# Performance work log

Hardware: AMD Instinct MI355X
Metric: run time of the kernel (lower is better)

The kernel has to match this reference:

```python
import jax, jax.numpy as jnp
import numpy as np
from jax import lax

B, T, A, L, H, FD = 32, 64, 6, 32, 128, 256


def setup_inputs() -> dict:
    key = jax.random.key(0)
    ks = jax.random.split(key, 24)
    rn = lambda k, s, sc: jax.random.normal(k, s, jnp.float32) * sc
    return {
        "states": rn(ks[0], (B, T, 3, 64, 64), 1.0),
        "actions": rn(ks[1], (B, T, A), 1.0),
        # CNN encoder params (scale ~ 1/sqrt(fan_in))
        "c1_w": rn(ks[2], (32, 3, 4, 4), 0.14), "c1_b": rn(ks[3], (32,), 0.01),
        "c2_w": rn(ks[4], (64, 32, 4, 4), 0.044), "c2_b": rn(ks[5], (64,), 0.01),
        "c3_w": rn(ks[6], (128, 64, 4, 4), 0.031), "c3_b": rn(ks[7], (128,), 0.01),
        "c4_w": rn(ks[8], (256, 128, 4, 4), 0.022), "c4_b": rn(ks[9], (256,), 0.01),
        "fc_w": rn(ks[10], (FD, 256 * 4 * 4), 0.0156), "fc_b": rn(ks[11], (FD,), 0.01),
        # GRUCell params (torch layout: W_ih (3H, in), W_hh (3H, H))
        "gru_wih": rn(ks[12], (3 * H, L + A), 0.16), "gru_whh": rn(ks[13], (3 * H, H), 0.088),
        "gru_bih": rn(ks[14], (3 * H,), 0.01), "gru_bhh": rn(ks[15], (3 * H,), 0.01),
        "prior_w": rn(ks[16], (2 * L, H), 0.088), "prior_b": rn(ks[17], (2 * L,), 0.01),
        "post_w": rn(ks[18], (2 * L, H + FD), 0.05), "post_b": rn(ks[19], (2 * L,), 0.01),
        # reparameterization noise (randn_like in torch), one per (b, t)
        "eps": rn(ks[20], (B, T, L), 1.0),
    }


def _conv(x, w, b):
    # Conv2d(k=4, stride=2, pad=1), NCHW/OIHW
    y = lax.conv_general_dilated(x, w, window_strides=(2, 2),
                                 padding=[(1, 1), (1, 1)],
                                 dimension_numbers=("NCHW", "OIHW", "NCHW"))
    return jax.nn.relu(y + b[None, :, None, None])


def _encode(x, c1_w, c1_b, c2_w, c2_b, c3_w, c3_b, c4_w, c4_b, fc_w, fc_b):
    # x: (N, 3, 64, 64) -> (N, FD)
    x = _conv(x, c1_w, c1_b)
    x = _conv(x, c2_w, c2_b)
    x = _conv(x, c3_w, c3_b)
    x = _conv(x, c4_w, c4_b)  # (N, 256, 4, 4)
    x = x.reshape(x.shape[0], -1)
    return x @ fc_w.T + fc_b


def _gru_cell(x, h, wih, whh, bih, bhh):
    gi = x @ wih.T + bih
    gh = h @ whh.T + bhh
    i_r, i_z, i_n = jnp.split(gi, 3, axis=-1)
    h_r, h_z, h_n = jnp.split(gh, 3, axis=-1)
    r = jax.nn.sigmoid(i_r + h_r)
    z = jax.nn.sigmoid(i_z + h_z)
    n = jnp.tanh(i_n + r * h_n)
    return (1.0 - z) * n + z * h


def reference(states, actions, c1_w, c1_b, c2_w, c2_b, c3_w, c3_b, c4_w, c4_b,
              fc_w, fc_b, gru_wih, gru_whh, gru_bih, gru_bhh,
              prior_w, prior_b, post_w, post_b, eps):
    b, t = states.shape[0], states.shape[1]
    # encoder has no recurrent dependency: encode all frames at once
    feats = _encode(states.reshape(b * t, *states.shape[2:]),
                    c1_w, c1_b, c2_w, c2_b, c3_w, c3_b, c4_w, c4_b,
                    fc_w, fc_b).reshape(b, t, -1)  # (B, T, FD)

    def step(carry, inp):
        h, z = carry
        a_t, f_t, e_t = inp
        h = _gru_cell(jnp.concatenate([z, a_t], -1), h,
                      gru_wih, gru_whh, gru_bih, gru_bhh)
        mu_p, lv_p = jnp.split(h @ prior_w.T + prior_b, 2, axis=-1)
        mu_q, lv_q = jnp.split(jnp.concatenate([h, f_t], -1) @ post_w.T + post_b, 2, axis=-1)
        z = mu_q + jnp.exp(0.5 * lv_q) * e_t
        return (h, z), (mu_p, lv_p, mu_q, lv_q, h, z)

    h0 = jnp.zeros((b, gru_whh.shape[1]), states.dtype)
    z0 = jnp.zeros((b, prior_w.shape[0] // 2), states.dtype)
    xs = (jnp.swapaxes(actions, 0, 1), jnp.swapaxes(feats, 0, 1),
          jnp.swapaxes(eps, 0, 1))
    _, ys = lax.scan(step, (h0, z0), xs)
    # (T, B, d) -> (B, T, d)
    return tuple(jnp.swapaxes(y, 0, 1) for y in ys)
```

## Files before the change

kernel.cpp:

```cpp
#include <hip/hip_runtime.h>
#include <math.h>

#define Bn 32
#define Tn 64
#define An 6
#define Ln 32
#define Hn 128
#define FDn 256
#define Nimg (Bn*Tn)

typedef __attribute__((ext_vector_type(8))) short frag_ab;
typedef __attribute__((ext_vector_type(4))) float frag_cd;
typedef _Float16 h2_t __attribute__((ext_vector_type(2)));

__device__ __forceinline__ float sigmoid_fast(float x){
  return __builtin_amdgcn_rcpf(1.f + __expf(-x));
}
__device__ __forceinline__ float tanh_fast(float x){
  float x2 = fminf(fmaxf(2.f*x, -30.f), 30.f);
  float e = __expf(x2);
  return (e - 1.f) * __builtin_amdgcn_rcpf(e + 1.f);
}

__device__ __forceinline__ unsigned short f2bf(float f){
  unsigned int u = __float_as_uint(f);
  unsigned int r = (u + 0x7fffu + ((u >> 16) & 1u)) >> 16;
  return (unsigned short)r;
}
__device__ __forceinline__ unsigned packh(float a, float b){
  union { h2_t h; unsigned u; } x;
  x.h = (h2_t){(_Float16)a, (_Float16)b};
  return x.u;
}
__device__ __forceinline__ float fdot2u(unsigned a, unsigned b, float c){
  union { unsigned u; h2_t h; } ua, ub;
  ua.u = a; ub.u = b;
#if __has_builtin(__builtin_amdgcn_fdot2)
  return __builtin_amdgcn_fdot2(ua.h, ub.h, c, false);
#else
  return c + (float)ua.h.x*(float)ub.h.x + (float)ua.h.y*(float)ub.h.y;
#endif
}
#define BAR_LDS() asm volatile("s_waitcnt lgkmcnt(0)\n\ts_barrier" ::: "memory")

__device__ __forceinline__ int swz_w(int r, int p){
  return ((r >> 4) << 9) + (p << 7) + ((((r & 15) ^ (p << 2))) << 3);
}
__device__ __forceinline__ int swz_r(int f, int l){
  return (f << 9) + ((l >> 4) << 7) + ((((l & 15) ^ ((l >> 4) << 2))) << 3);
}

__global__ void __launch_bounds__(256)
states_nhwc_kernel(const float* __restrict__ src, unsigned short* __restrict__ dst)
{
  int idx = blockIdx.x*256 + threadIdx.x;
  int n = idx >> 12, pix = idx & 4095;
  const float* s = src + (size_t)n*3*4096 + pix;
  union { unsigned short e[4]; uint2 v; } u;
  u.e[0] = f2bf(s[0]); u.e[1] = f2bf(s[4096]); u.e[2] = f2bf(s[8192]); u.e[3] = 0;
  *(uint2*)(dst + (size_t)idx*4) = u.v;
}

#define WHH4_U 24576
#define PO4_U  (64*53*4)
#define SCAN_U (WHH4_U + PO4_U)

__global__ void __launch_bounds__(256)
prep2_kernel(const float* __restrict__ c1w, const float* __restrict__ c2w,
             const float* __restrict__ c3w, const float* __restrict__ c4w,
             const float* __restrict__ fcw,
             const float* __restrict__ gwhh, const float* __restrict__ gwih,
             const float* __restrict__ prw,  const float* __restrict__ pow_,
             unsigned short* __restrict__ w1p, unsigned short* __restrict__ w2p,
             unsigned short* __restrict__ w3p, unsigned short* __restrict__ w4p,
             unsigned short* __restrict__ wfcp,
             unsigned* __restrict__ g_scan, unsigned* __restrict__ g_wih2,
             unsigned* __restrict__ g_pr2)
{
  const int bid = blockIdx.x, tid = threadIdx.x;
  if (bid < 128){
    int idx = bid*256+tid;
    int k = idx >> 9, r = idx & 511, tap = r >> 5, c = r & 31;
    w2p[idx] = f2bf(c2w[k*512 + c*16 + tap]);
  } else if (bid < 640){
    int idx = (bid-128)*256+tid;
    int k = idx >> 10, r = idx & 1023, tap = r >> 6, c = r & 63;
    w3p[idx] = f2bf(c3w[k*1024 + c*16 + tap]);
  } else if (bid < 2688){
    int idx = (bid-640)*256+tid;
    int k = idx >> 11, r = idx & 2047, tap = r >> 7, c = r & 127;
    w4p[idx] = f2bf(c4w[k*2048 + c*16 + tap]);
  } else if (bid < 6784){
    int idx = (bid-2688)*256+tid;
    int o = idx >> 12, r = idx & 4095, sp = r >> 8, c = r & 255;
    wfcp[idx] = f2bf(fcw[o*4096 + c*16 + sp]);
  } else if (bid < 6792){
    int idx = (bid-6784)*256+tid;
    int k = idx >> 6, r = idx & 63, tap = r >> 2, c = r & 3;
    w1p[idx] = (c < 3) ? f2bf(c1w[k*48 + c*16 + tap]) : (unsigned short)0;
  } else if (bid < 6888){
    int idx = (bid-6792)*256+tid;
    int q = idx & 3, r2 = idx >> 2;
    int k8 = r2 / 384, i = r2 - k8*384;
    int k = 8*k8 + 2*q;
    g_scan[idx] = packh(gwhh[i*128 + k], gwhh[i*128 + k + 1]);
  } else if (bid < 6917){
    int idx = (bid-6888)*256+tid;
    if (idx < 19*384){
      int c = idx / 384, i = idx - c*384;
      g_wih2[idx] = packh(gwih[i*38 + 2*c], gwih[i*38 + 2*c + 1]);
    }
  } else if (bid < 6933){
    int idx = (bid-6917)*256+tid;
    int o = idx >> 6, c = idx & 63;
    g_pr2[idx] = packh(prw[o*128 + 2*c], prw[o*128 + 2*c + 1]);
  } else {
    int idx = (bid-6933)*256+tid;
    if (idx < 64*192){
      int o = idx / 192, r2 = idx - o*192;
      int u = r2 >> 2, q = r2 & 3;
      int j = u / 12, kk = u - j*12;
      int k = 96*j + 8*kk + 2*q;
      g_scan[WHH4_U + (o*53 + j*13 + kk)*4 + q] =
        packh(pow_[o*384 + k], pow_[o*384 + k + 1]);
    }
  }
}

template<int Cin, int IN, int Kout, int OUT, int BN, int LOG_SPB>
__global__ void __launch_bounds__(256)
convN_mfma(const unsigned short* __restrict__ in,
           const unsigned short* __restrict__ wB,
           const float* __restrict__ bias,
           unsigned short* __restrict__ out)
{
  constexpr int SPB = OUT*OUT;
  constexpr int KD  = 16*Cin;
  constexpr int NCH = KD/32;
  constexpr int NFN = BN/32;
  constexpr int BFR = BN/16;
  constexpr int BSL = (BN*4 + 255)/256;
  __shared__ __align__(16) unsigned short Alds[2][8*512];
  __shared__ __align__(16) unsigned short Blds[2][BFR*512];

  const int tid = threadIdx.x;
  const int wave = tid >> 6, lane = tid & 63;
  const unsigned m0 = blockIdx.x * 128;
  const int n0 = blockIdx.y * BN;

  const int p = tid & 3;
  const unsigned short* baseA[2]; int oyA[2], oxA[2]; int AdstI[2];
#pragma unroll
  for (int h = 0; h < 2; h++){
    int r = (tid >> 2) + h*64;
    unsigned m = m0 + r;
    int nimg = m >> LOG_SPB;
    int sp = m & (SPB - 1);
    oyA[h] = sp / OUT; oxA[h] = sp & (OUT - 1);
    baseA[h] = in + (size_t)nimg * IN * IN * Cin;
    AdstI[h] = swz_w(r, p);
  }

  const unsigned short* BsrcH[BSL]; int BdstIH[BSL]; bool bActH[BSL];
#pragma unroll
  for (int h = 0; h < BSL; h++){
    int bn = (tid >> 2) + h*64, pb = tid & 3;
    bActH[h] = bn < BN;
    BsrcH[h] = wB + (size_t)(n0 + bn)*KD + pb*8;
    BdstIH[h] = swz_w(bn, pb);
  }

  const int mhalf = wave >> 1, nhalf = wave & 1;
  frag_cd acc[4][NFN];
#pragma unroll
  for (int i = 0; i < 4; i++)
#pragma unroll
    for (int j = 0; j < NFN; j++) acc[i][j] = (frag_cd){0.f,0.f,0.f,0.f};

  auto loadA = [&](int kt, int h) -> uint4 {
    if constexpr (Cin >= 32){
      constexpr int CPT = Cin/32;
      int tap = kt / CPT;
      int c0 = (kt - tap*CPT)*32;
      int kh = tap >> 2, kw = tap & 3;
      int iy = 2*oyA[h] - 1 + kh;
      int ix = 2*oxA[h] - 1 + kw;
      uint4 v = {0u,0u,0u,0u};
      if ((unsigned)iy < (unsigned)IN && (unsigned)ix < (unsigned)IN)
        v = *(const uint4*)(baseA[h] + ((iy*IN + ix)*Cin + c0 + p*8));
      return v;
    } else {
      int kh = kt*2 + (p >> 1);
      int kw0 = (p & 1)*2;
      int iy = 2*oyA[h] - 1 + kh;
      int ix0 = 2*oxA[h] - 1 + kw0;
      union { uint2 u2[2]; uint4 u4; } v; v.u4 = (uint4){0u,0u,0u,0u};
      bool iyok = (unsigned)iy < (unsigned)IN;
      const unsigned short* rowp = baseA[h] + iy*IN*4;
#pragma unroll
      for (int d = 0; d < 2; d++){
        int ix = ix0 + d;
        if (iyok && (unsigned)ix < (unsigned)IN) v.u2[d] = *(const uint2*)(rowp + ix*4);
      }
      return v.u4;
    }
  };

  const int rdoff = swz_r(0, lane);

  uint4 aR0 = loadA(0,0), aR1 = loadA(0,1);
  uint4 bR[BSL];
#pragma unroll
  for (int h = 0; h < BSL; h++)
    bR[h] = bActH[h] ? *(const uint4*)BsrcH[h] : (uint4){0u,0u,0u,0u};
  *(uint4*)&Alds[0][AdstI[0]] = aR0;
  *(uint4*)&Alds[0][AdstI[1]] = aR1;
#pragma unroll
  for (int h = 0; h < BSL; h++)
    if (bActH[h]) *(uint4*)&Blds[0][BdstIH[h]] = bR[h];
  if (NCH > 1){
    aR0 = loadA(1,0); aR1 = loadA(1,1);
#pragma unroll
    for (int h = 0; h < BSL; h++)
      if (bActH[h]) bR[h] = *(const uint4*)(BsrcH[h] + 32);
  }
  BAR_LDS();

#pragma unroll 2
  for (int kt = 0; kt < NCH; kt++){
    const int cur = kt & 1, nxt = cur ^ 1;
    if (kt + 1 < NCH){
      *(uint4*)&Alds[nxt][AdstI[0]] = aR0;
      *(uint4*)&Alds[nxt][AdstI[1]] = aR1;
#pragma unroll
      for (int h = 0; h < BSL; h++)
        if (bActH[h]) *(uint4*)&Blds[nxt][BdstIH[h]] = bR[h];
      if (kt + 2 < NCH){
        aR0 = loadA(kt+2, 0);
        aR1 = loadA(kt+2, 1);
#pragma unroll
        for (int h = 0; h < BSL; h++)
          if (bActH[h]) bR[h] = *(const uint4*)(BsrcH[h] + (kt+2)*32);
      }
    }
    frag_ab a[4], bf[NFN];
#pragma unroll
    for (int i = 0; i < 4; i++)
      a[i] = *(const frag_ab*)&Alds[cur][(((mhalf<<2) + i) << 9) + rdoff];
#pragma unroll
    for (int j = 0; j < NFN; j++)
      bf[j] = *(const frag_ab*)&Blds[cur][((nhalf*NFN + j) << 9) + rdoff];
#pragma unroll
    for (int i = 0; i < 4; i++)
#pragma unroll
      for (int j = 0; j < NFN; j++)
        acc[i][j] = __builtin_amdgcn_mfma_f32_16x16x32_bf16(a[i], bf[j], acc[i][j], 0, 0, 0);
    BAR_LDS();
  }

  const unsigned mb = m0 + mhalf*64 + ((lane >> 4) << 2);
#pragma unroll
  for (int j = 0; j < NFN; j++){
    const int kg = n0 + nhalf*(NFN*16) + j*16 + (lane & 15);
    const float bv = bias[kg];
#pragma unroll
    for (int i = 0; i < 4; i++){
#pragma unroll
      for (int r = 0; r < 4; r++){
        unsigned mg = mb + i*16 + r;
        out[(size_t)mg*Kout + kg] = f2bf(fmaxf(acc[i][j][r] + bv, 0.f));
      }
    }
  }
}

__global__ void __launch_bounds__(256)
fc_mfma2(const unsigned short* __restrict__ A, const unsigned short* __restrict__ wB,
         const float* __restrict__ bias, float* __restrict__ outF)
{
  constexpr int KD = 4096, NCH = KD/32;
  __shared__ __align__(16) unsigned short Alds[2][4*512];
  __shared__ __align__(16) unsigned short Blds[2][4*512];

  const int tid = threadIdx.x, wave = tid >> 6, lane = tid & 63;
  const int m0 = blockIdx.x * 64, n0 = blockIdx.y * 64;
  const int r = tid >> 2, pc = tid & 3;
  const unsigned short* Asrc = A + (size_t)(m0 + r)*KD + pc*8;
  const unsigned short* Bsrc = wB + (size_t)(n0 + r)*KD + pc*8;
  const int wI = swz_w(r, pc);
  const int mh = wave >> 1, nh = wave & 1;
  const int rdoff = swz_r(0, lane);

  frag_cd acc[2][2];
#pragma unroll
  for (int i = 0; i < 2; i++)
#pragma unroll
    for (int j = 0; j < 2; j++) acc[i][j] = (frag_cd){0.f,0.f,0.f,0.f};

  uint4 aP = *(const uint4*)Asrc, bP = *(const uint4*)Bsrc;
  *(uint4*)&Alds[0][wI] = aP;
  *(uint4*)&Blds[0][wI] = bP;
  aP = *(const uint4*)(Asrc + 32);
  bP = *(const uint4*)(Bsrc + 32);
  BAR_LDS();

#pragma unroll 2
  for (int kt = 0; kt < NCH; kt++){
    const int cur = kt & 1, nxt = cur ^ 1;
    if (kt + 1 < NCH){
      *(uint4*)&Alds[nxt][wI] = aP;
      *(uint4*)&Blds[nxt][wI] = bP;
      if (kt + 2 < NCH){
        aP = *(const uint4*)(Asrc + (kt+2)*32);
        bP = *(const uint4*)(Bsrc + (kt+2)*32);
      }
    }
    frag_ab a[2], b[2];
#pragma unroll
    for (int i = 0; i < 2; i++) a[i] = *(const frag_ab*)&Alds[cur][(((mh<<1)+i) << 9) + rdoff];
#pragma unroll
    for (int j = 0; j < 2; j++) b[j] = *(const frag_ab*)&Blds[cur][(((nh<<1)+j) << 9) + rdoff];
#pragma unroll
    for (int i = 0; i < 2; i++)
#pragma unroll
      for (int j = 0; j < 2; j++)
        acc[i][j] = __builtin_amdgcn_mfma_f32_16x16x32_bf16(a[i], b[j], acc[i][j], 0, 0, 0);
    BAR_LDS();
  }

  const int mb = m0 + mh*32 + ((lane >> 4) << 2);
#pragma unroll
  for (int j = 0; j < 2; j++){
    const int kg = n0 + nh*32 + j*16 + (lane & 15);
    const float bv = bias[kg];
#pragma unroll
    for (int i = 0; i < 2; i++)
#pragma unroll
      for (int rr = 0; rr < 4; rr++)
        outF[(size_t)(mb + i*16 + rr)*256 + kg] = acc[i][j][rr] + bv;
  }
}

__global__ void __launch_bounds__(384)
rssm_scan4(const float* __restrict__ actions, const float* __restrict__ feats,
           const float* __restrict__ eps,
           const unsigned* __restrict__ g_scan,
           const unsigned* __restrict__ g_wih2,
           const unsigned* __restrict__ g_pr2,
           const float* __restrict__ bih,  const float* __restrict__ bhh,
           const float* __restrict__ prior_b, const float* __restrict__ post_b,
           float* __restrict__ out)
{
  __shared__ __align__(16) _Float16 sh_hfh[384];
  __shared__ __align__(16) _Float16 sh_xh[40];
  __shared__ __align__(16) float sh_gi[384];
  __shared__ __align__(16) float sh_gh[384];

  const int b = blockIdx.x, tid = threadIdx.x;

  uint4 whhr[16];
  {
    const uint4* src = (const uint4*)g_scan;
#pragma unroll
    for (int k8 = 0; k8 < 16; k8++) whhr[k8] = src[k8*384 + tid];
  }
  unsigned wih[19];
#pragma unroll
  for (int c = 0; c < 19; c++) wih[c] = g_wih2[c*384 + tid];

  unsigned prw[32];
  float prb = 0.f;
  if (tid < 128){
    const unsigned* src = g_pr2 + (tid >> 1)*64 + (tid & 1)*32;
#pragma unroll
    for (int c = 0; c < 32; c++) prw[c] = src[c];
    prb = prior_b[tid >> 1];
  }

  int om = 0, pj = 0, o_p = 0; bool is_mu = false; float pob = 0.f;
  uint4 pww[12];
  if (tid >= 128){
    const int tt = tid - 128;
    om = tt >> 2; pj = tt & 3;
    o_p = (om >> 1) + (om & 1)*32;
    is_mu = !(om & 1);
    pob = post_b[o_p];
    const uint4* src = (const uint4*)(g_scan + WHH4_U) + o_p*53 + pj*13;
#pragma unroll
    for (int kk = 0; kk < 12; kk++) pww[kk] = src[kk];
  }

  const float bih_i = bih[tid], bhh_i = bhh[tid];
  float hreg = 0.f;

  {
    const int bt0 = b*Tn;
    if (tid < Hn) sh_hfh[tid] = (_Float16)0.f;
    if (tid < Ln) sh_xh[tid] = (_Float16)0.f;
    if (tid >= 32 && tid < 38) sh_xh[tid] = (_Float16)actions[(size_t)bt0*An + (tid-32)];
    if (tid >= 64 && tid < 320) sh_hfh[128 + tid - 64] = (_Float16)feats[(size_t)bt0*FDn + (tid-64)];
  }
  __syncthreads();

  const uint4* H4   = (const uint4*)sh_hfh;
  const unsigned* X2 = (const unsigned*)sh_xh;

  const int OFF_MUP = 0;
  const int OFF_LVP = Bn*Tn*Ln;
  const int OFF_MUQ = 2*Bn*Tn*Ln;
  const int OFF_LVQ = 3*Bn*Tn*Ln;
  const int OFF_H   = 4*Bn*Tn*Ln;
  const int OFF_Z   = 4*Bn*Tn*Ln + Bn*Tn*Hn;

  float freg = 0.f, areg = 0.f, epsr = 0.f;

  for (int t = 0; t < Tn; t++){
    const int bt = b*Tn + t;

    if (t > 0 && tid >= 64 && tid < 320) sh_hfh[128 + tid - 64] = (_Float16)freg;
    if (t < Tn-1){
      if (tid >= 64 && tid < 320) freg = feats[(size_t)(bt+1)*FDn + (tid-64)];
      if (tid >= 320 && tid < 326) areg = actions[(size_t)(bt+1)*An + (tid-320)];
    }
    if (tid >= 128 && ((tid-128)&7) == 0) epsr = eps[(size_t)bt*Ln + ((tid-128)>>3)];

    {
      float a0 = bih_i, a1 = 0.f;
#pragma unroll
      for (int c = 0; c < 19; c += 2) a0 = fdot2u(wih[c], X2[c], a0);
#pragma unroll
      for (int c = 1; c < 19; c += 2) a1 = fdot2u(wih[c], X2[c], a1);
      sh_gi[tid] = a0 + a1;

      float g0 = bhh_i, g1 = 0.f, g2 = 0.f, g3 = 0.f;
#pragma unroll
      for (int k8 = 0; k8 < 16; k8++){
        uint4 w = whhr[k8];
        uint4 h = H4[k8];
        g0 = fdot2u(w.x, h.x, g0);
        g1 = fdot2u(w.y, h.y, g1);
        g2 = fdot2u(w.z, h.z, g2);
        g3 = fdot2u(w.w, h.w, g3);
      }
      sh_gh[tid] = (g0 + g1) + (g2 + g3);
    }
    BAR_LDS();

    if (tid < Hn){
      const float r  = sigmoid_fast(sh_gi[tid]       + sh_gh[tid]);
      const float zg = sigmoid_fast(sh_gi[Hn  + tid] + sh_gh[Hn  + tid]);
      const float nn = tanh_fast(fmaf(r, sh_gh[2*Hn + tid], sh_gi[2*Hn + tid]));
      hreg = (1.f - zg)*nn + zg*hreg;
      sh_hfh[tid] = (_Float16)hreg;
      out[OFF_H + (size_t)bt*Hn + tid] = hreg;
    }
    if (t < Tn-1 && tid >= 320 && tid < 326) sh_xh[32 + tid - 320] = (_Float16)areg;
    BAR_LDS();

    if (tid < 128){
      const int j = tid & 1;
      float a0 = 0.f, a1 = 0.f, a2 = 0.f, a3 = 0.f;
#pragma unroll
      for (int c4 = 0; c4 < 8; c4++){
        uint4 h = H4[8*j + c4];
        a0 = fdot2u(prw[4*c4+0], h.x, a0);
        a1 = fdot2u(prw[4*c4+1], h.y, a1);
        a2 = fdot2u(prw[4*c4+2], h.z, a2);
        a3 = fdot2u(prw[4*c4+3], h.w, a3);
      }
      float p = (a0 + a1) + (a2 + a3);
      p += __shfl_xor(p, 1);
      if (j == 0){
        const int o = tid >> 1;
        p += prb;
        if (o < Ln) out[OFF_MUP + (size_t)bt*Ln + o] = p;
        else        out[OFF_LVP + (size_t)bt*Ln + (o - Ln)] = p;
      }
    } else {
      float a0 = 0.f, a1 = 0.f, a2 = 0.f, a3 = 0.f;
#pragma unroll
      for (int kk = 0; kk < 12; kk++){
        uint4 w = pww[kk];
        uint4 h = H4[pj*12 + kk];
        a0 = fdot2u(w.x, h.x, a0);
        a1 = fdot2u(w.y, h.y, a1);
        a2 = fdot2u(w.z, h.z, a2);
        a3 = fdot2u(w.w, h.w, a3);
      }
      float p = (a0 + a1) + (a2 + a3);
      p += __shfl_xor(p, 1);
      p += __shfl_xor(p, 2);
      p += pob;
      const float q_part = __shfl_xor(p, 4);
      if (pj == 0){
        if (is_mu){
          const int o = om >> 1;
          out[OFF_MUQ + (size_t)bt*Ln + o] = p;
          const float zz = fmaf(__expf(0.5f*q_part), epsr, p);
          sh_xh[o] = (_Float16)zz;
          out[OFF_Z + (size_t)bt*Ln + o] = zz;
        } else {
          out[OFF_LVQ + (size_t)bt*Ln + (o_p - Ln)] = p;
        }
      }
    }
    BAR_LDS();
  }
}

extern "C" void kernel_launch(void* const* d_in, const int* in_sizes, int n_in,
                              void* d_out, int out_size, void* d_ws, size_t ws_size,
                              hipStream_t stream)
{
  const float* states = (const float*)d_in[0];
  const float* actions= (const float*)d_in[1];
  const float* c1_w = (const float*)d_in[2];  const float* c1_b = (const float*)d_in[3];
  const float* c2_w = (const float*)d_in[4];  const float* c2_b = (const float*)d_in[5];
  const float* c3_w = (const float*)d_in[6];  const float* c3_b = (const float*)d_in[7];
  const float* c4_w = (const float*)d_in[8];  const float* c4_b = (const float*)d_in[9];
  const float* fc_w = (const float*)d_in[10]; const float* fc_b = (const float*)d_in[11];
  const float* gwih = (const float*)d_in[12]; const float* gwhh = (const float*)d_in[13];
  const float* gbih = (const float*)d_in[14]; const float* gbhh = (const float*)d_in[15];
  const float* pr_w = (const float*)d_in[16]; const float* pr_b = (const float*)d_in[17];
  const float* po_w = (const float*)d_in[18]; const float* po_b = (const float*)d_in[19];
  const float* eps  = (const float*)d_in[20];

  char* p = (char*)d_ws;
  auto alloc = [&](size_t bytes){ char* r = p; p += (bytes + 255) & ~255ULL; return r; };

  unsigned short* statesB = (unsigned short*)alloc((size_t)Nimg*4096*4*2);
  unsigned short* act1    = (unsigned short*)alloc((size_t)Nimg*1024*32*2);
  unsigned short* act2    = (unsigned short*)alloc((size_t)Nimg*256*64*2);
  unsigned short* act3    = (unsigned short*)alloc((size_t)Nimg*64*128*2);
  unsigned short* act4    = (unsigned short*)alloc((size_t)Nimg*16*256*2);
  float*          feats   = (float*)alloc((size_t)Nimg*FDn*4);
  unsigned short* w1p     = (unsigned short*)alloc(32*64*2);
  unsigned short* w2p     = (unsigned short*)alloc((size_t)64*512*2);
  unsigned short* w3p     = (unsigned short*)alloc((size_t)128*1024*2);
  unsigned short* w4p     = (unsigned short*)alloc((size_t)256*2048*2);
  unsigned short* wfcp    = (unsigned short*)alloc((size_t)256*4096*2);
  unsigned* g_scan = (unsigned*)alloc((size_t)SCAN_U*4);
  unsigned* g_wih2 = (unsigned*)alloc((size_t)19*384*4);
  unsigned* g_pr2  = (unsigned*)alloc((size_t)64*64*4);

  states_nhwc_kernel<<<Nimg*4096/256, 256, 0, stream>>>(states, statesB);
  prep2_kernel<<<6981, 256, 0, stream>>>(c1_w, c2_w, c3_w, c4_w, fc_w,
                                         gwhh, gwih, pr_w, po_w,
                                         w1p, w2p, w3p, w4p, wfcp,
                                         g_scan, g_wih2, g_pr2);

  convN_mfma<4,64,32,32,32,10>  <<< dim3(Nimg*1024/128, 1), 256, 0, stream >>>(statesB, w1p, c1_b, act1);
  convN_mfma<32,32,64,16,64,8>  <<< dim3(Nimg*256/128, 1), 256, 0, stream >>>(act1, w2p, c2_b, act2);
  convN_mfma<64,16,128,8,128,6> <<< dim3(Nimg*64/128, 1), 256, 0, stream >>>(act2, w3p, c3_b, act3);
  convN_mfma<128,8,256,4,128,4> <<< dim3(Nimg*16/128, 2), 256, 0, stream >>>(act3, w4p, c4_b, act4);

  fc_mfma2<<< dim3(Nimg/64, 4), 256, 0, stream >>>(act4, wfcp, fc_b, feats);

  rssm_scan4<<< Bn, 384, 0, stream >>>(actions, feats, eps,
                                       g_scan, g_wih2, g_pr2,
                                       gbih, gbhh, pr_b, po_b, (float*)d_out);
}
```

Baseline: 564.4 us.

## Hoist action and feature projections out of RSSM scan into parallel kernels

The non-recurrent parts of the GRU input projection (actions·W_ih + b_ih) and of the posterior projection (feats·W_post + b_post) are now computed for all timesteps up front by two new parallel kernels. This shortens the serial per-step work in the scan, which now only contracts the recurrent z and h inputs. The scan also broadcasts h to every thread's registers with readlane and gives the prior and posterior heads one wave each with 64-wide weight rows held in registers. In exchange it adds two kernel launches, extra global buffers, and much higher register pressure in the scan kernel.

```diff
diff --git a/kernel.cpp b/kernel.cpp
--- a/kernel.cpp
+++ b/kernel.cpp
@@ -60,10 +60,6 @@
   u.e[0] = f2bf(s[0]); u.e[1] = f2bf(s[4096]); u.e[2] = f2bf(s[8192]); u.e[3] = 0;
   *(uint2*)(dst + (size_t)idx*4) = u.v;
 }
-
-#define WHH4_U 24576
-#define PO4_U  (64*53*4)
-#define SCAN_U (WHH4_U + PO4_U)
 
 __global__ void __launch_bounds__(256)
 prep2_kernel(const float* __restrict__ c1w, const float* __restrict__ c2w,
@@ -74,8 +70,8 @@
              unsigned short* __restrict__ w1p, unsigned short* __restrict__ w2p,
              unsigned short* __restrict__ w3p, unsigned short* __restrict__ w4p,
              unsigned short* __restrict__ wfcp,
-             unsigned* __restrict__ g_scan, unsigned* __restrict__ g_wih2,
-             unsigned* __restrict__ g_pr2)
+             unsigned* __restrict__ g_whh2, unsigned* __restrict__ g_wihz,
+             unsigned* __restrict__ g_pr2,  unsigned* __restrict__ g_po2)
 {
   const int bid = blockIdx.x, tid = threadIdx.x;
   if (bid < 128){
@@ -100,30 +96,73 @@
     w1p[idx] = (c < 3) ? f2bf(c1w[k*48 + c*16 + tap]) : (unsigned short)0;
   } else if (bid < 6888){
     int idx = (bid-6792)*256+tid;
-    int q = idx & 3, r2 = idx >> 2;
-    int k8 = r2 / 384, i = r2 - k8*384;
-    int k = 8*k8 + 2*q;
-    g_scan[idx] = packh(gwhh[i*128 + k], gwhh[i*128 + k + 1]);
-  } else if (bid < 6917){
+    int c = idx / 384, i = idx - c*384;
+    g_whh2[idx] = packh(gwhh[i*128 + 2*c], gwhh[i*128 + 2*c + 1]);
+  } else if (bid < 6912){
     int idx = (bid-6888)*256+tid;
-    if (idx < 19*384){
-      int c = idx / 384, i = idx - c*384;
-      g_wih2[idx] = packh(gwih[i*38 + 2*c], gwih[i*38 + 2*c + 1]);
-    }
-  } else if (bid < 6933){
-    int idx = (bid-6917)*256+tid;
-    int o = idx >> 6, c = idx & 63;
+    int c = idx / 384, i = idx - c*384;
+    g_wihz[idx] = packh(gwih[i*38 + 2*c], gwih[i*38 + 2*c + 1]);
+  } else if (bid < 6928){
+    int idx = (bid-6912)*256+tid;
+    int c = idx >> 6, o = idx & 63;
     g_pr2[idx] = packh(prw[o*128 + 2*c], prw[o*128 + 2*c + 1]);
   } else {
-    int idx = (bid-6933)*256+tid;
-    if (idx < 64*192){
-      int o = idx / 192, r2 = idx - o*192;
-      int u = r2 >> 2, q = r2 & 3;
-      int j = u / 12, kk = u - j*12;
-      int k = 96*j + 8*kk + 2*q;
-      g_scan[WHH4_U + (o*53 + j*13 + kk)*4 + q] =
-        packh(pow_[o*384 + k], pow_[o*384 + k + 1]);
-    }
+    int idx = (bid-6928)*256+tid;
+    int c = idx >> 6, o = idx & 63;
+    g_po2[idx] = packh(pow_[o*384 + 2*c], pow_[o*384 + 2*c + 1]);
+  }
+}
+
+__global__ void __launch_bounds__(384)
+gia_kernel(const float* __restrict__ actions, const float* __restrict__ gwih,
+           const float* __restrict__ bih, float* __restrict__ GIA)
+{
+  const int tid = threadIdx.x;
+  const int bt0 = blockIdx.x * 8;
+  __shared__ float ash[48];
+  if (tid < 48) ash[tid] = actions[(size_t)bt0*6 + tid];
+  float w6[6];
+#pragma unroll
+  for (int k = 0; k < 6; k++) w6[k] = gwih[tid*38 + 32 + k];
+  const float bv = bih[tid];
+  __syncthreads();
+#pragma unroll
+  for (int r = 0; r < 8; r++){
+    float v = bv;
+#pragma unroll
+    for (int k = 0; k < 6; k++) v = fmaf(ash[r*6+k], w6[k], v);
+    GIA[(size_t)(bt0 + r)*384 + tid] = v;
+  }
+}
+
+__global__ void __launch_bounds__(256)
+pof_kernel(const float* __restrict__ feats, const float* __restrict__ po_w,
+           const float* __restrict__ po_b, float* __restrict__ POF)
+{
+  const int tid = threadIdx.x;
+  const int bt0 = blockIdx.x * 8;
+  __shared__ __align__(16) float fsh[8*256];
+  const float4* fsrc = (const float4*)(feats + (size_t)bt0*256);
+  ((float4*)fsh)[tid]       = fsrc[tid];
+  ((float4*)fsh)[tid + 256] = fsrc[tid + 256];
+  __syncthreads();
+  const float4* w4 = (const float4*)po_w;
+  const float4* f4 = (const float4*)fsh;
+#pragma unroll
+  for (int i = 0; i < 2; i++){
+    int item = tid + i*256;
+    int row = item >> 6, o = item & 63;
+    float4 acc = {0.f,0.f,0.f,0.f};
+#pragma unroll 8
+    for (int k = 0; k < 64; k++){
+      float4 wv = w4[o*96 + 32 + k];
+      float4 fv = f4[row*64 + k];
+      acc.x = fmaf(wv.x, fv.x, acc.x);
+      acc.y = fmaf(wv.y, fv.y, acc.y);
+      acc.z = fmaf(wv.z, fv.z, acc.z);
+      acc.w = fmaf(wv.w, fv.w, acc.w);
+    }
+    POF[(size_t)(bt0 + row)*64 + o] = (acc.x + acc.y) + (acc.z + acc.w) + po_b[o];
   }
 }
 
@@ -342,68 +381,49 @@
 }
 
 __global__ void __launch_bounds__(384)
-rssm_scan4(const float* __restrict__ actions, const float* __restrict__ feats,
-           const float* __restrict__ eps,
-           const unsigned* __restrict__ g_scan,
-           const unsigned* __restrict__ g_wih2,
-           const unsigned* __restrict__ g_pr2,
-           const float* __restrict__ bih,  const float* __restrict__ bhh,
-           const float* __restrict__ prior_b, const float* __restrict__ post_b,
-           float* __restrict__ out)
-{
-  __shared__ __align__(16) _Float16 sh_hfh[384];
-  __shared__ __align__(16) _Float16 sh_xh[40];
-  __shared__ __align__(16) float sh_gi[384];
-  __shared__ __align__(16) float sh_gh[384];
+rssm_scan5(const unsigned* __restrict__ g_whh2, const unsigned* __restrict__ g_wihz,
+           const unsigned* __restrict__ g_pr2,  const unsigned* __restrict__ g_po2,
+           const float* __restrict__ GIA, const float* __restrict__ POF,
+           const float* __restrict__ eps, const float* __restrict__ bhh,
+           const float* __restrict__ pr_b, float* __restrict__ out)
+{
+  __shared__ __align__(16) _Float16 sh_h[128];
+  __shared__ __align__(16) _Float16 sh_z[32];
+  __shared__ float sh_gi[384];
+  __shared__ float sh_gh[384];
 
   const int b = blockIdx.x, tid = threadIdx.x;
-
-  uint4 whhr[16];
-  {
-    const uint4* src = (const uint4*)g_scan;
-#pragma unroll
-    for (int k8 = 0; k8 < 16; k8++) whhr[k8] = src[k8*384 + tid];
-  }
-  unsigned wih[19];
-#pragma unroll
-  for (int c = 0; c < 19; c++) wih[c] = g_wih2[c*384 + tid];
-
-  unsigned prw[32];
-  float prb = 0.f;
-  if (tid < 128){
-    const unsigned* src = g_pr2 + (tid >> 1)*64 + (tid & 1)*32;
-#pragma unroll
-    for (int c = 0; c < 32; c++) prw[c] = src[c];
-    prb = prior_b[tid >> 1];
-  }
-
-  int om = 0, pj = 0, o_p = 0; bool is_mu = false; float pob = 0.f;
-  uint4 pww[12];
-  if (tid >= 128){
-    const int tt = tid - 128;
-    om = tt >> 2; pj = tt & 3;
-    o_p = (om >> 1) + (om & 1)*32;
-    is_mu = !(om & 1);
-    pob = post_b[o_p];
-    const uint4* src = (const uint4*)(g_scan + WHH4_U) + o_p*53 + pj*13;
-#pragma unroll
-    for (int kk = 0; kk < 12; kk++) pww[kk] = src[kk];
-  }
-
-  const float bih_i = bih[tid], bhh_i = bhh[tid];
-  float hreg = 0.f;
-
-  {
-    const int bt0 = b*Tn;
-    if (tid < Hn) sh_hfh[tid] = (_Float16)0.f;
-    if (tid < Ln) sh_xh[tid] = (_Float16)0.f;
-    if (tid >= 32 && tid < 38) sh_xh[tid] = (_Float16)actions[(size_t)bt0*An + (tid-32)];
-    if (tid >= 64 && tid < 320) sh_hfh[128 + tid - 64] = (_Float16)feats[(size_t)bt0*FDn + (tid-64)];
-  }
-  __syncthreads();
-
-  const uint4* H4   = (const uint4*)sh_hfh;
-  const unsigned* X2 = (const unsigned*)sh_xh;
+  const int wv = tid >> 6, lane = tid & 63;
+
+  unsigned whh2[64];
+#pragma unroll
+  for (int c = 0; c < 64; c++) whh2[c] = g_whh2[c*384 + tid];
+  unsigned wihz[16];
+#pragma unroll
+  for (int c = 0; c < 16; c++) wihz[c] = g_wihz[c*384 + tid];
+  const float bhh_i = bhh[tid];
+
+  unsigned wpx[64];
+  float prbr = 0.f;
+  if (wv == 0){
+#pragma unroll
+    for (int c = 0; c < 64; c++) wpx[c] = g_pr2[c*64 + lane];
+    prbr = pr_b[lane];
+  } else if (wv == 1){
+#pragma unroll
+    for (int c = 0; c < 64; c++) wpx[c] = g_po2[c*64 + lane];
+  }
+
+  unsigned hsu[64];
+#pragma unroll
+  for (int c = 0; c < 64; c++) hsu[c] = 0u;
+
+  if (tid < 128) sh_h[tid] = (_Float16)0.f;
+  if (tid < 32)  sh_z[tid] = (_Float16)0.f;
+
+  float GIAr = GIA[(size_t)(b*64)*384 + tid];
+  float POFr = (wv == 1) ? POF[(size_t)(b*64)*64 + lane] : 0.f;
+  float epsr = (wv == 1 && lane < 32) ? eps[(size_t)(b*64)*32 + lane] : 0.f;
 
   const int OFF_MUP = 0;
   const int OFF_LVP = Bn*Tn*Ln;
@@ -412,96 +432,88 @@
   const int OFF_H   = 4*Bn*Tn*Ln;
   const int OFF_Z   = 4*Bn*Tn*Ln + Bn*Tn*Hn;
 
-  float freg = 0.f, areg = 0.f, epsr = 0.f;
+  float hreg = 0.f;
+  __syncthreads();
 
   for (int t = 0; t < Tn; t++){
-    const int bt = b*Tn + t;
-
-    if (t > 0 && tid >= 64 && tid < 320) sh_hfh[128 + tid - 64] = (_Float16)freg;
-    if (t < Tn-1){
-      if (tid >= 64 && tid < 320) freg = feats[(size_t)(bt+1)*FDn + (tid-64)];
-      if (tid >= 320 && tid < 326) areg = actions[(size_t)(bt+1)*An + (tid-320)];
-    }
-    if (tid >= 128 && ((tid-128)&7) == 0) epsr = eps[(size_t)bt*Ln + ((tid-128)>>3)];
+    const size_t bt = (size_t)b*64 + t;
 
     {
-      float a0 = bih_i, a1 = 0.f;
-#pragma unroll
-      for (int c = 0; c < 19; c += 2) a0 = fdot2u(wih[c], X2[c], a0);
-#pragma unroll
-      for (int c = 1; c < 19; c += 2) a1 = fdot2u(wih[c], X2[c], a1);
-      sh_gi[tid] = a0 + a1;
+      const uint4* Z4 = (const uint4*)sh_z;
+      uint4 z0 = Z4[0], z1 = Z4[1], z2 = Z4[2], z3 = Z4[3];
+      float a0 = GIAr, a1 = 0.f, a2 = 0.f, a3 = 0.f;
+      a0 = fdot2u(wihz[0],  z0.x, a0); a1 = fdot2u(wihz[1],  z0.y, a1);
+      a2 = fdot2u(wihz[2],  z0.z, a2); a3 = fdot2u(wihz[3],  z0.w, a3);
+      a0 = fdot2u(wihz[4],  z1.x, a0); a1 = fdot2u(wihz[5],  z1.y, a1);
+      a2 = fdot2u(wihz[6],  z1.z, a2); a3 = fdot2u(wihz[7],  z1.w, a3);
+      a0 = fdot2u(wihz[8],  z2.x, a0); a1 = fdot2u(wihz[9],  z2.y, a1);
+      a2 = fdot2u(wihz[10], z2.z, a2); a3 = fdot2u(wihz[11], z2.w, a3);
+      a0 = fdot2u(wihz[12], z3.x, a0); a1 = fdot2u(wihz[13], z3.y, a1);
+      a2 = fdot2u(wihz[14], z3.z, a2); a3 = fdot2u(wihz[15], z3.w, a3);
 
       float g0 = bhh_i, g1 = 0.f, g2 = 0.f, g3 = 0.f;
 #pragma unroll
-      for (int k8 = 0; k8 < 16; k8++){
-        uint4 w = whhr[k8];
-        uint4 h = H4[k8];
-        g0 = fdot2u(w.x, h.x, g0);
-        g1 = fdot2u(w.y, h.y, g1);
-        g2 = fdot2u(w.z, h.z, g2);
-        g3 = fdot2u(w.w, h.w, g3);
-      }
+      for (int c = 0; c < 64; c += 4){
+        g0 = fdot2u(whh2[c],   hsu[c],   g0);
+        g1 = fdot2u(whh2[c+1], hsu[c+1], g1);
+        g2 = fdot2u(whh2[c+2], hsu[c+2], g2);
+        g3 = fdot2u(whh2[c+3], hsu[c+3], g3);
+      }
+      sh_gi[tid] = (a0 + a1) + (a2 + a3);
       sh_gh[tid] = (g0 + g1) + (g2 + g3);
     }
+    if (t < Tn-1) GIAr = GIA[(bt+1)*384 + tid];
     BAR_LDS();
 
-    if (tid < Hn){
+    if (tid < 128){
       const float r  = sigmoid_fast(sh_gi[tid]       + sh_gh[tid]);
-      const float zg = sigmoid_fast(sh_gi[Hn  + tid] + sh_gh[Hn  + tid]);
-      const float nn = tanh_fast(fmaf(r, sh_gh[2*Hn + tid], sh_gi[2*Hn + tid]));
+      const float zg = sigmoid_fast(sh_gi[128 + tid] + sh_gh[128 + tid]);
+      const float nn = tanh_fast(fmaf(r, sh_gh[256 + tid], sh_gi[256 + tid]));
       hreg = (1.f - zg)*nn + zg*hreg;
-      sh_hfh[tid] = (_Float16)hreg;
-      out[OFF_H + (size_t)bt*Hn + tid] = hreg;
-    }
-    if (t < Tn-1 && tid >= 320 && tid < 326) sh_xh[32 + tid - 320] = (_Float16)areg;
+      sh_h[tid] = (_Float16)hreg;
+      out[OFF_H + bt*128 + tid] = hreg;
+    }
     BAR_LDS();
 
-    if (tid < 128){
-      const int j = tid & 1;
-      float a0 = 0.f, a1 = 0.f, a2 = 0.f, a3 = 0.f;
-#pragma unroll
-      for (int c4 = 0; c4 < 8; c4++){
-        uint4 h = H4[8*j + c4];
-        a0 = fdot2u(prw[4*c4+0], h.x, a0);
-        a1 = fdot2u(prw[4*c4+1], h.y, a1);
-        a2 = fdot2u(prw[4*c4+2], h.z, a2);
-        a3 = fdot2u(prw[4*c4+3], h.w, a3);
-      }
-      float p = (a0 + a1) + (a2 + a3);
-      p += __shfl_xor(p, 1);
-      if (j == 0){
-        const int o = tid >> 1;
-        p += prb;
-        if (o < Ln) out[OFF_MUP + (size_t)bt*Ln + o] = p;
-        else        out[OFF_LVP + (size_t)bt*Ln + (o - Ln)] = p;
-      }
-    } else {
-      float a0 = 0.f, a1 = 0.f, a2 = 0.f, a3 = 0.f;
-#pragma unroll
-      for (int kk = 0; kk < 12; kk++){
-        uint4 w = pww[kk];
-        uint4 h = H4[pj*12 + kk];
-        a0 = fdot2u(w.x, h.x, a0);
-        a1 = fdot2u(w.y, h.y, a1);
-        a2 = fdot2u(w.z, h.z, a2);
-        a3 = fdot2u(w.w, h.w, a3);
-      }
-      float p = (a0 + a1) + (a2 + a3);
-      p += __shfl_xor(p, 1);
-      p += __shfl_xor(p, 2);
-      p += pob;
-      const float q_part = __shfl_xor(p, 4);
-      if (pj == 0){
-        if (is_mu){
-          const int o = om >> 1;
-          out[OFF_MUQ + (size_t)bt*Ln + o] = p;
-          const float zz = fmaf(__expf(0.5f*q_part), epsr, p);
-          sh_xh[o] = (_Float16)zz;
-          out[OFF_Z + (size_t)bt*Ln + o] = zz;
-        } else {
-          out[OFF_LVQ + (size_t)bt*Ln + (o_p - Ln)] = p;
-        }
+    {
+      unsigned hv = ((const unsigned*)sh_h)[lane];
+#pragma unroll
+      for (int c = 0; c < 64; c++) hsu[c] = __builtin_amdgcn_readlane(hv, c);
+    }
+    if (wv == 0){
+      float p0 = prbr, p1 = 0.f, p2 = 0.f, p3 = 0.f;
+#pragma unroll
+      for (int c = 0; c < 64; c += 4){
+        p0 = fdot2u(wpx[c],   hsu[c],   p0);
+        p1 = fdot2u(wpx[c+1], hsu[c+1], p1);
+        p2 = fdot2u(wpx[c+2], hsu[c+2], p2);
+        p3 = fdot2u(wpx[c+3], hsu[c+3], p3);
+      }
+      const float p = (p0 + p1) + (p2 + p3);
+      if (lane < 32) out[OFF_MUP + bt*32 + lane] = p;
+      else           out[OFF_LVP + bt*32 + (lane - 32)] = p;
+    } else if (wv == 1){
+      float p0 = POFr, p1 = 0.f, p2 = 0.f, p3 = 0.f;
+#pragma unroll
+      for (int c = 0; c < 64; c += 4){
+        p0 = fdot2u(wpx[c],   hsu[c],   p0);
+        p1 = fdot2u(wpx[c+1], hsu[c+1], p1);
+        p2 = fdot2u(wpx[c+2], hsu[c+2], p2);
+        p3 = fdot2u(wpx[c+3], hsu[c+3], p3);
+      }
+      const float p = (p0 + p1) + (p2 + p3);
+      const float q = __shfl_xor(p, 32);
+      if (lane < 32){
+        out[OFF_MUQ + bt*32 + lane] = p;
+        const float zz = fmaf(__expf(0.5f*q), epsr, p);
+        sh_z[lane] = (_Float16)zz;
+        out[OFF_Z + bt*32 + lane] = zz;
+      } else {
+        out[OFF_LVQ + bt*32 + (lane - 32)] = p;
+      }
+      if (t < Tn-1){
+        POFr = POF[(bt+1)*64 + lane];
+        if (lane < 32) epsr = eps[(bt+1)*32 + lane];
       }
     }
     BAR_LDS();
@@ -539,15 +551,19 @@
   unsigned short* w3p     = (unsigned short*)alloc((size_t)128*1024*2);
   unsigned short* w4p     = (unsigned short*)alloc((size_t)256*2048*2);
   unsigned short* wfcp    = (unsigned short*)alloc((size_t)256*4096*2);
-  unsigned* g_scan = (unsigned*)alloc((size_t)SCAN_U*4);
-  unsigned* g_wih2 = (unsigned*)alloc((size_t)19*384*4);
-  unsigned* g_pr2  = (unsigned*)alloc((size_t)64*64*4);
+  unsigned* g_whh2 = (unsigned*)alloc((size_t)24576*4);
+  unsigned* g_wihz = (unsigned*)alloc((size_t)6144*4);
+  unsigned* g_pr2  = (unsigned*)alloc((size_t)4096*4);
+  unsigned* g_po2  = (unsigned*)alloc((size_t)4096*4);
+  float*    GIAb   = (float*)alloc((size_t)786432*4);
+  float*    POFb   = (float*)alloc((size_t)Nimg*64*4);
 
   states_nhwc_kernel<<<Nimg*4096/256, 256, 0, stream>>>(states, statesB);
-  prep2_kernel<<<6981, 256, 0, stream>>>(c1_w, c2_w, c3_w, c4_w, fc_w,
+  prep2_kernel<<<6944, 256, 0, stream>>>(c1_w, c2_w, c3_w, c4_w, fc_w,
                                          gwhh, gwih, pr_w, po_w,
                                          w1p, w2p, w3p, w4p, wfcp,
-                                         g_scan, g_wih2, g_pr2);
+                                         g_whh2, g_wihz, g_pr2, g_po2);
+  gia_kernel<<<Nimg/8, 384, 0, stream>>>(actions, gwih, gbih, GIAb);
 
   convN_mfma<4,64,32,32,32,10>  <<< dim3(Nimg*1024/128, 1), 256, 0, stream >>>(statesB, w1p, c1_b, act1);
   convN_mfma<32,32,64,16,64,8>  <<< dim3(Nimg*256/128, 1), 256, 0, stream >>>(act1, w2p, c2_b, act2);
@@ -555,8 +571,8 @@
   convN_mfma<128,8,256,4,128,4> <<< dim3(Nimg*16/128, 2), 256, 0, stream >>>(act3, w4p, c4_b, act4);
 
   fc_mfma2<<< dim3(Nimg/64, 4), 256, 0, stream >>>(act4, wfcp, fc_b, feats);
-
-  rssm_scan4<<< Bn, 384, 0, stream >>>(actions, feats, eps,
-                                       g_scan, g_wih2, g_pr2,
-                                       gbih, gbhh, pr_b, po_b, (float*)d_out);
-}
+  pof_kernel<<< Nimg/8, 256, 0, stream >>>(feats, po_w, po_b, POFb);
+
+  rssm_scan5<<< Bn, 384, 0, stream >>>(g_whh2, g_wihz, g_pr2, g_po2,
+                                       GIAb, POFb, eps, gbhh, pr_b, (float*)d_out);
+}
```

After: 572.7 us. Within noise of the previous version (+1.5%).
